# Performance work log

Hardware: AMD Instinct MI355X
Metric: run time of the kernel (lower is better)

## Reference

```python
import jax, jax.numpy as jnp
import numpy as np

D_MODEL = 1024
HEADS = 16
D_K = D_MODEL // HEADS
D_FF = 4096
B, S = 2, 2048
EPS = 1e-5


def setup_inputs() -> dict:
    key = jax.random.key(0)
    ks = jax.random.split(key, 16)
    sc_att = 1.0 / np.sqrt(D_MODEL)
    sc_ff1 = 1.0 / np.sqrt(D_MODEL)
    sc_ff2 = 1.0 / np.sqrt(D_FF)
    return {
        "input": jax.random.normal(ks[0], (B, S, D_MODEL), jnp.float32),
        "mask": jnp.ones((B, 1, 1, S), jnp.int32),
        # stacked per-head projections: [H, D_MODEL, D_K]
        "Wq": jax.random.normal(ks[1], (HEADS, D_MODEL, D_K), jnp.float32) * sc_att,
        "bq": jax.random.normal(ks[2], (HEADS, D_K), jnp.float32) * 0.01,
        "Wk": jax.random.normal(ks[3], (HEADS, D_MODEL, D_K), jnp.float32) * sc_att,
        "bk": jax.random.normal(ks[4], (HEADS, D_K), jnp.float32) * 0.01,
        "Wv": jax.random.normal(ks[5], (HEADS, D_MODEL, D_K), jnp.float32) * sc_att,
        "bv": jax.random.normal(ks[6], (HEADS, D_K), jnp.float32) * 0.01,
        "Wo": jax.random.normal(ks[7], (D_MODEL, D_MODEL), jnp.float32) * sc_att,
        "bo": jax.random.normal(ks[8], (D_MODEL,), jnp.float32) * 0.01,
        "ln1_g": jnp.ones((D_MODEL,), jnp.float32),
        "ln1_b": jnp.zeros((D_MODEL,), jnp.float32),
        "ln2_g": jnp.ones((D_MODEL,), jnp.float32),
        "ln2_b": jnp.zeros((D_MODEL,), jnp.float32),
        "W1": jax.random.normal(ks[9], (D_MODEL, D_FF), jnp.float32) * sc_ff1,
        "b1": jax.random.normal(ks[10], (D_FF,), jnp.float32) * 0.01,
        "W2": jax.random.normal(ks[11], (D_FF, D_MODEL), jnp.float32) * sc_ff2,
        "b2": jax.random.normal(ks[12], (D_MODEL,), jnp.float32) * 0.01,
    }


def _layernorm(x, g, b):
    mu = jnp.mean(x, axis=-1, keepdims=True)
    var = jnp.mean(jnp.square(x - mu), axis=-1, keepdims=True)
    return (x - mu) * jax.lax.rsqrt(var + EPS) * g + b


def reference(input, mask, Wq, bq, Wk, bk, Wv, bv, Wo, bo,
              ln1_g, ln1_b, ln2_g, ln2_b, W1, b1, W2, b2):
    x = input
    # per-head projections, stacked: [B,H,S,D_K]
    q = jnp.einsum('bsd,hdk->bhsk', x, Wq) + bq[None, :, None, :]
    k = jnp.einsum('bsd,hdk->bhsk', x, Wk) + bk[None, :, None, :]
    v = jnp.einsum('bsd,hdk->bhsk', x, Wv) + bv[None, :, None, :]
    scores = jnp.einsum('bhqk,bhsk->bhqs', q, k) / np.sqrt(D_K)  # [B,H,S,S]
    scores = jnp.where(mask == 0, jnp.float32(-1e9), scores)
    attn = jax.nn.softmax(scores, axis=-1)
    ctx = jnp.einsum('bhqs,bhsk->bhqk', attn, v)  # [B,H,S,D_K]
    # concat heads along feature dim (head h occupies slice h*D_K:(h+1)*D_K)
    ctx = jnp.transpose(ctx, (0, 2, 1, 3)).reshape(B, S, D_MODEL)
    att_out = ctx @ Wo + bo
    h = _layernorm(x + att_out, ln1_g, ln1_b)
    ff = jax.nn.relu(h @ W1 + b1) @ W2 + b2
    return _layernorm(h + ff, ln2_g, ln2_b)
```

## Files before the change

### kernel.cpp

```cpp
#include <hip/hip_runtime.h>
#include <cstdint>
#include <cstddef>

typedef unsigned short u16;
typedef unsigned int   u32;
typedef unsigned short u16x4 __attribute__((ext_vector_type(4)));
typedef unsigned short u16x8 __attribute__((ext_vector_type(8)));
typedef unsigned int   u32x2 __attribute__((ext_vector_type(2)));
typedef __bf16 bf16x8 __attribute__((ext_vector_type(8)));
typedef float f32x4 __attribute__((ext_vector_type(4)));

#define MFMA16(a, b, c) __builtin_amdgcn_mfma_f32_16x16x32_bf16((a), (b), (c), 0, 0, 0)
#define WAIT_VM0() __builtin_amdgcn_s_waitcnt(0x0F70)
#define BARRIER()  __builtin_amdgcn_s_barrier()

__device__ __forceinline__ float bf2f(u16 h) {
  union { unsigned u; float f; } v; v.u = ((unsigned)h) << 16; return v.f;
}
__device__ __forceinline__ u16 f2bf(float f) {
  union { float f; unsigned u; } v; v.f = f;
  unsigned r = v.u + 0x7fffu + ((v.u >> 16) & 1u);
  return (u16)(r >> 16);
}
__device__ __forceinline__ void gll16(const u16* g, u16* l) {
  __builtin_amdgcn_global_load_lds(
      (const __attribute__((address_space(1))) void*)g,
      (__attribute__((address_space(3))) void*)l, 16, 0, 0);
}
__device__ __forceinline__ float fast_exp2(float x) {
#if __has_builtin(__builtin_amdgcn_exp2f)
  return __builtin_amdgcn_exp2f(x);
#else
  return exp2f(x);
#endif
}

__global__ __launch_bounds__(256) void transpose_qkv(
    const float* __restrict__ Wq, const float* __restrict__ Wk,
    const float* __restrict__ Wv, u16* __restrict__ outb) {
  __shared__ u16 tile[32][33];
  const int z = blockIdx.z;
  const int which = z >> 4, h = z & 15;
  const float* in = (which == 0 ? Wq : (which == 1 ? Wk : Wv)) + (size_t)h * 1024 * 64;
  u16* out = outb + ((size_t)which * 1024 + h * 64) * 1024;
  const int tx = threadIdx.x & 31, ty = threadIdx.x >> 5;
  const int r0 = blockIdx.y * 32, c0 = blockIdx.x * 32;
  #pragma unroll
  for (int i = 0; i < 32; i += 8)
    tile[ty + i][tx] = f2bf(in[(size_t)(r0 + ty + i) * 64 + c0 + tx]);
  __syncthreads();
  #pragma unroll
  for (int i = 0; i < 32; i += 8)
    out[(size_t)(c0 + ty + i) * 1024 + r0 + tx] = tile[tx][ty + i];
}

__global__ __launch_bounds__(256) void transpose_w(
    const float* __restrict__ Wo, const float* __restrict__ W1,
    const float* __restrict__ W2, u16* __restrict__ Wo_t,
    u16* __restrict__ W1_t, u16* __restrict__ W2_t) {
  __shared__ u16 tile[32][33];
  const int id = blockIdx.x;
  const float* in; u16* outp; int R, C, cx, ry;
  if (id < 1024)      { in = Wo; outp = Wo_t; R = 1024; C = 1024; cx = id & 31;  ry = id >> 5; }
  else if (id < 5120) { int t = id - 1024; in = W1; outp = W1_t; R = 1024; C = 4096; cx = t & 127; ry = t >> 7; }
  else                { int t = id - 5120; in = W2; outp = W2_t; R = 4096; C = 1024; cx = t & 31;  ry = t >> 5; }
  const int tx = threadIdx.x & 31, ty = threadIdx.x >> 5;
  const int r0 = ry * 32, c0 = cx * 32;
  #pragma unroll
  for (int i = 0; i < 32; i += 8)
    tile[ty + i][tx] = f2bf(in[(size_t)(r0 + ty + i) * C + c0 + tx]);
  __syncthreads();
  #pragma unroll
  for (int i = 0; i < 32; i += 8)
    outp[(size_t)(c0 + ty + i) * R + r0 + tx] = tile[tx][ty + i];
}

__global__ __launch_bounds__(256) void prep_small(
    const float* __restrict__ bq, const float* __restrict__ bk,
    const float* __restrict__ bv, const int* __restrict__ mask,
    float* __restrict__ biasq, float* __restrict__ madd2) {
  int i = blockIdx.x * 256 + threadIdx.x;
  if (i < 3072) {
    biasq[i] = (i < 1024) ? bq[i] : (i < 2048 ? bk[i - 1024] : bv[i - 2048]);
  } else if (i < 7168) {
    int j = i - 3072;
    madd2[j] = mask[j] ? -23.083120f : -1.442695e9f;
  }
}

__global__ __launch_bounds__(256) void cvt_x(
    const float* __restrict__ in, u16* __restrict__ out, int n) {
  int i = (blockIdx.x * 256 + threadIdx.x) * 4;
  if (i >= n) return;
  const float4 v = *(const float4*)&in[i];
  u16x4 o;
  o[0] = f2bf(v.x); o[1] = f2bf(v.y); o[2] = f2bf(v.z); o[3] = f2bf(v.w);
  *(u16x4*)&out[i] = o;
}

template <int MODE>
__global__ __launch_bounds__(256) void gemm_bt(
    const u16* __restrict__ A, const u16* __restrict__ Bt,
    const float* __restrict__ bias, u16* __restrict__ C,
    int M, int N, int K) {
  __shared__ __align__(16) u16 As[2][128 * 32];
  __shared__ __align__(16) u16 Bs[2][128 * 32];
  const int tid = threadIdx.x;
  const int lane = tid & 63;
  const int wave = tid >> 6;
  const int m0 = blockIdx.y * 128;
  const int n0 = blockIdx.x * 128;
  const int kz = (MODE == 2) ? blockIdx.z : 0;
  const int Keff = (MODE == 2) ? (K >> 1) : K;
  const int kbase = kz * Keff;
  const int wr = (wave >> 1) * 64;
  const int wc = (wave & 1) * 64;
  const int lrow = lane & 15;
  const int quad = lane >> 4;

  const int srow = lane >> 2;
  const int scol = (lane & 3) * 8;
  const u16* gA1 = &A[(size_t)(m0 + wave * 16 + srow) * K + kbase + scol];
  const u16* gA2 = &A[(size_t)(m0 + 64 + wave * 16 + srow) * K + kbase + scol];
  const u16* gB1 = &Bt[(size_t)(n0 + wave * 16 + srow) * K + kbase + scol];
  const u16* gB2 = &Bt[(size_t)(n0 + 64 + wave * 16 + srow) * K + kbase + scol];
  const int so1 = (wave * 16) * 32;
  const int so2 = (wave * 16 + 64) * 32;
  u16* Cw = (MODE == 2) ? (C + (size_t)kz * M * N) : C;

  f32x4 acc[4][4];
  #pragma unroll
  for (int i = 0; i < 4; ++i)
    #pragma unroll
    for (int j = 0; j < 4; ++j)
      acc[i][j] = (f32x4){0.f, 0.f, 0.f, 0.f};

  gll16(gA1, &As[0][so1]);
  gll16(gA2, &As[0][so2]);
  gll16(gB1, &Bs[0][so1]);
  gll16(gB2, &Bs[0][so2]);

  const int nIter = Keff >> 5;
  for (int it = 0; it < nIter; ++it) {
    const int cur = it & 1;
    WAIT_VM0();
    BARRIER();
    const int k1 = (it + 1) << 5;
    if (k1 < Keff) {
      gll16(gA1 + k1, &As[cur ^ 1][so1]);
      gll16(gA2 + k1, &As[cur ^ 1][so2]);
      gll16(gB1 + k1, &Bs[cur ^ 1][so1]);
      gll16(gB2 + k1, &Bs[cur ^ 1][so2]);
    }
    bf16x8 af[4], bfr[4];
    #pragma unroll
    for (int i = 0; i < 4; ++i) {
      af[i]  = *(const bf16x8*)&As[cur][(wr + i * 16 + lrow) * 32 + quad * 8];
      bfr[i] = *(const bf16x8*)&Bs[cur][(wc + i * 16 + lrow) * 32 + quad * 8];
    }
    #pragma unroll
    for (int fr = 0; fr < 4; ++fr)
      #pragma unroll
      for (int fc = 0; fc < 4; ++fc)
        acc[fr][fc] = MFMA16(af[fr], bfr[fc], acc[fr][fc]);
  }

  #pragma unroll
  for (int fr = 0; fr < 4; ++fr) {
    int rowb = m0 + wr + fr * 16 + quad * 4;
    #pragma unroll
    for (int fc = 0; fc < 4; ++fc) {
      int col = n0 + wc + fc * 16 + lrow;
      float bv = (MODE == 2) ? 0.f : bias[col];
      #pragma unroll
      for (int r = 0; r < 4; ++r) {
        float v = acc[fr][fc][r] + bv;
        if (MODE == 1) v = fmaxf(v, 0.f);
        Cw[(size_t)(rowb + r) * N + col] = f2bf(v);
      }
    }
  }
}

__global__ __launch_bounds__(256) void attn_kernel(
    const u16* __restrict__ xqkv, const float* __restrict__ madd2,
    u16* __restrict__ opart, float* __restrict__ lpart) {
  __shared__ __align__(16) u16 Ks[64][72];
  __shared__ __align__(16) u16 Vt[64][136];
  __shared__ __align__(16) u16 Ps[4][2][16][72];
  const int tid = threadIdx.x;
  const int lane = tid & 63;
  const int wave = tid >> 6;
  const int lrow = lane & 15;
  const int quad = lane >> 4;
  const int b = blockIdx.z >> 1, kz = blockIdx.z & 1;
  const int h = blockIdx.y;
  const int qb = blockIdx.x * 128 + wave * 16;
  const u16* Qp = xqkv + (size_t)b * 2048 * 3072 + h * 64;
  const u16* Kp = Qp + 1024;
  const u16* Vp = Qp + 2048;
  const float S2 = 0.18033688f;
  const int sbeg = kz * 1024, send = sbeg + 1024;

  bf16x8 qa[2][2];
  #pragma unroll
  for (int t = 0; t < 2; ++t) {
    qa[t][0] = *(const bf16x8*)&Qp[(size_t)(qb + t * 64 + lrow) * 3072 + quad * 8];
    qa[t][1] = *(const bf16x8*)&Qp[(size_t)(qb + t * 64 + lrow) * 3072 + 32 + quad * 8];
  }

  f32x4 o[2][4];
  #pragma unroll
  for (int t = 0; t < 2; ++t)
    #pragma unroll
    for (int i = 0; i < 4; ++i) o[t][i] = (f32x4){0.f, 0.f, 0.f, 0.f};
  float rsum[2] = {0.f, 0.f};

  const int ks_row = tid >> 3, ks_col = (tid & 7) * 8;
  const int v_dg = tid >> 4;
  const int v_kp = tid & 15;
  const float* maddb = madd2 + b * 2048;

  u16x8 kreg[2];
  u16x4 va[2], vb[2];
  #pragma unroll
  for (int sh = 0; sh < 2; ++sh) {
    kreg[sh] = *(const u16x8*)&Kp[(size_t)(sbeg + sh * 32 + ks_row) * 3072 + ks_col];
    va[sh] = *(const u16x4*)&Vp[(size_t)(sbeg + sh * 32 + 2 * v_kp) * 3072 + v_dg * 4];
    vb[sh] = *(const u16x4*)&Vp[(size_t)(sbeg + sh * 32 + 2 * v_kp + 1) * 3072 + v_dg * 4];
  }

  for (int s0 = sbeg; s0 < send; s0 += 64) {
    __syncthreads();
    #pragma unroll
    for (int sh = 0; sh < 2; ++sh) {
      *(u16x8*)&Ks[sh * 32 + ks_row][ks_col] = kreg[sh];
      #pragma unroll
      for (int j = 0; j < 4; ++j) {
        u32 pk = ((u32)vb[sh][j] << 16) | (u32)va[sh][j];
        *(u32*)&Vt[v_dg * 4 + j][sh * 32 + 2 * v_kp] = pk;
      }
    }
    __syncthreads();
    if (s0 + 64 < send) {
      #pragma unroll
      for (int sh = 0; sh < 2; ++sh) {
        int sb = s0 + 64 + sh * 32;
        kreg[sh] = *(const u16x8*)&Kp[(size_t)(sb + ks_row) * 3072 + ks_col];
        va[sh] = *(const u16x4*)&Vp[(size_t)(sb + 2 * v_kp) * 3072 + v_dg * 4];
        vb[sh] = *(const u16x4*)&Vp[(size_t)(sb + 2 * v_kp + 1) * 3072 + v_dg * 4];
      }
    }

    bf16x8 kf[4][2], vf[4][2];
    #pragma unroll
    for (int kb = 0; kb < 4; ++kb) {
      kf[kb][0] = *(const bf16x8*)&Ks[kb * 16 + lrow][quad * 8];
      kf[kb][1] = *(const bf16x8*)&Ks[kb * 16 + lrow][32 + quad * 8];
    }
    #pragma unroll
    for (int nb = 0; nb < 4; ++nb) {
      vf[nb][0] = *(const bf16x8*)&Vt[nb * 16 + lrow][quad * 8];
      vf[nb][1] = *(const bf16x8*)&Vt[nb * 16 + lrow][32 + quad * 8];
    }

    #pragma unroll
    for (int t = 0; t < 2; ++t) {
      #pragma unroll
      for (int kb = 0; kb < 4; ++kb) {
        f32x4 z = (f32x4){0.f, 0.f, 0.f, 0.f};
        z = MFMA16(kf[kb][0], qa[t][0], z);
        z = MFMA16(kf[kb][1], qa[t][1], z);
        f32x4 m4 = *(const f32x4*)&maddb[s0 + kb * 16 + quad * 4];
        u32 pb[4];
        #pragma unroll
        for (int r = 0; r < 4; ++r) {
          float p = fast_exp2(fmaf(z[r], S2, m4[r]));
          rsum[t] += p;
          union { float f; u32 u; } cv; cv.f = p;
          pb[r] = cv.u + 0x8000u;
        }
        u32x2 w2;
        w2[0] = __builtin_amdgcn_perm(pb[1], pb[0], 0x07060302);
        w2[1] = __builtin_amdgcn_perm(pb[3], pb[2], 0x07060302);
        *(u32x2*)&Ps[wave][t][lrow][kb * 16 + quad * 4] = w2;
      }
      #pragma unroll
      for (int kh = 0; kh < 2; ++kh) {
        bf16x8 pa = *(const bf16x8*)&Ps[wave][t][lrow][kh * 32 + quad * 8];
        #pragma unroll
        for (int nb = 0; nb < 4; ++nb)
          o[t][nb] = MFMA16(pa, vf[nb][kh], o[t][nb]);
      }
    }
  }

  u16* ob = opart + (size_t)kz * 4194304;
  float* lb = lpart + (size_t)kz * 65536 + ((size_t)b * 16 + h) * 2048;
  #pragma unroll
  for (int t = 0; t < 2; ++t) {
    float rs = rsum[t];
    rs += __shfl_xor(rs, 16, 64);
    rs += __shfl_xor(rs, 32, 64);
    if (lane < 16) lb[qb + t * 64 + lane] = rs;
    #pragma unroll
    for (int r = 0; r < 4; ++r) {
      int q = qb + t * 64 + quad * 4 + r;
      #pragma unroll
      for (int nb = 0; nb < 4; ++nb)
        ob[((size_t)b * 2048 + q) * 1024 + h * 64 + nb * 16 + lrow] =
            f2bf(o[t][nb][r]);
    }
  }
}

__global__ __launch_bounds__(256) void attn_combine(
    const u16* __restrict__ opart, const float* __restrict__ lpart,
    u16* __restrict__ ctx) {
  const int t = blockIdx.x;
  const int b = t >> 11, q = t & 2047;
  const int tid = threadIdx.x;
  const size_t base = (size_t)t * 1024;
  #pragma unroll
  for (int i = 0; i < 4; ++i) {
    int c = i * 256 + tid;
    int h = c >> 6;
    float l = lpart[((size_t)b * 16 + h) * 2048 + q] +
              lpart[65536 + ((size_t)b * 16 + h) * 2048 + q];
    float o = bf2f(opart[base + c]) + bf2f(opart[4194304 + base + c]);
    ctx[base + c] = f2bf(o / fmaxf(l, 1e-30f));
  }
}

template <int IN_BF, int OUT_BF>
__global__ __launch_bounds__(256) void add_ln2p(
    const void* __restrict__ xa_, const u16* __restrict__ p0,
    const u16* __restrict__ p1, const float* __restrict__ cb,
    const float* __restrict__ g, const float* __restrict__ bb,
    void* __restrict__ outp_) {
  __shared__ float red[8];
  const int tid = threadIdx.x;
  const size_t base = (size_t)blockIdx.x * 1024;
  const float* xf = (const float*)xa_;
  const u16*   xb = (const u16*)xa_;
  float v[4];
  float s = 0.f;
  #pragma unroll
  for (int i = 0; i < 4; ++i) {
    int c = i * 256 + tid;
    float xv = IN_BF ? bf2f(xb[base + c]) : xf[base + c];
    v[i] = xv + bf2f(p0[base + c]) + bf2f(p1[base + c]) + cb[c];
    s += v[i];
  }
  #pragma unroll
  for (int off = 32; off > 0; off >>= 1) s += __shfl_down(s, off, 64);
  if ((tid & 63) == 0) red[tid >> 6] = s;
  __syncthreads();
  float mean = (red[0] + red[1] + red[2] + red[3]) * (1.f / 1024.f);
  float s2 = 0.f;
  #pragma unroll
  for (int i = 0; i < 4; ++i) { float d = v[i] - mean; s2 += d * d; }
  #pragma unroll
  for (int off = 32; off > 0; off >>= 1) s2 += __shfl_down(s2, off, 64);
  if ((tid & 63) == 0) red[4 + (tid >> 6)] = s2;
  __syncthreads();
  float var = (red[4] + red[5] + red[6] + red[7]) * (1.f / 1024.f);
  float rstd = rsqrtf(var + 1e-5f);
  #pragma unroll
  for (int i = 0; i < 4; ++i) {
    int c = i * 256 + tid;
    float r = (v[i] - mean) * rstd * g[c] + bb[c];
    if (OUT_BF) ((u16*)outp_)[base + c] = f2bf(r);
    else        ((float*)outp_)[base + c] = r;
  }
}

extern "C" void kernel_launch(void* const* d_in, const int* in_sizes, int n_in,
                              void* d_out, int out_size, void* d_ws, size_t ws_size,
                              hipStream_t stream) {
  (void)in_sizes; (void)n_in; (void)out_size; (void)ws_size;
  const float* x    = (const float*)d_in[0];
  const int*   mask = (const int*)d_in[1];
  const float* Wq   = (const float*)d_in[2];
  const float* bq   = (const float*)d_in[3];
  const float* Wk   = (const float*)d_in[4];
  const float* bk   = (const float*)d_in[5];
  const float* Wv   = (const float*)d_in[6];
  const float* bv   = (const float*)d_in[7];
  const float* Wo   = (const float*)d_in[8];
  const float* bo   = (const float*)d_in[9];
  const float* ln1g = (const float*)d_in[10];
  const float* ln1b = (const float*)d_in[11];
  const float* ln2g = (const float*)d_in[12];
  const float* ln2b = (const float*)d_in[13];
  const float* W1   = (const float*)d_in[14];
  const float* b1   = (const float*)d_in[15];
  const float* W2   = (const float*)d_in[16];
  const float* b2   = (const float*)d_in[17];
  float* out = (float*)d_out;

  char* ws = (char*)d_ws;
  float* lpart  = (float*)(ws + 0);
  u16*   fp     = (u16*)(ws + 0);
  u16*   Wqkv_t = (u16*)(ws + 0);
  u16*   Wo_t   = (u16*)(ws + 6291456);
  u16*   W1_t   = (u16*)(ws + 8388608);
  u16*   W2_t   = (u16*)(ws + 16777216);
  u16*   xqkv   = (u16*)(ws + 25165824);
  u16*   wp     = (u16*)(ws + 25165824);
  u16*   xb     = (u16*)(ws + 50331648);
  u16*   ctx    = (u16*)(ws + 50331648);
  u16*   opart  = (u16*)(ws + 58720256);
  u16*   hbuf   = (u16*)(ws + 58720256);
  u16*   ff1    = (u16*)(ws + 25165824);
  float* biasq  = (float*)(ws + 75497472);
  float* madd2  = (float*)(ws + 75509760);

  prep_small<<<28, 256, 0, stream>>>(bq, bk, bv, mask, biasq, madd2);
  transpose_qkv<<<dim3(2, 32, 48), 256, 0, stream>>>(Wq, Wk, Wv, Wqkv_t);
  transpose_w<<<9216, 256, 0, stream>>>(Wo, W1, W2, Wo_t, W1_t, W2_t);
  cvt_x<<<4096, 256, 0, stream>>>(x, xb, 4194304);

  gemm_bt<0><<<dim3(24, 32), 256, 0, stream>>>(xb, Wqkv_t, biasq, xqkv,
                                               4096, 3072, 1024);
  attn_kernel<<<dim3(16, 16, 4), 256, 0, stream>>>(xqkv, madd2, opart, lpart);
  attn_combine<<<4096, 256, 0, stream>>>(opart, lpart, ctx);
  gemm_bt<2><<<dim3(8, 32, 2), 256, 0, stream>>>(ctx, Wo_t, nullptr, wp,
                                                 4096, 1024, 1024);
  add_ln2p<0, 1><<<4096, 256, 0, stream>>>(x, wp, wp + 4194304, bo,
                                           ln1g, ln1b, hbuf);
  gemm_bt<1><<<dim3(32, 32), 256, 0, stream>>>(hbuf, W1_t, b1, ff1,
                                               4096, 4096, 1024);
  gemm_bt<2><<<dim3(8, 32, 2), 256, 0, stream>>>(ff1, W2_t, nullptr, fp,
                                                 4096, 1024, 4096);
  add_ln2p<1, 0><<<4096, 256, 0, stream>>>(hbuf, fp, fp + 4194304, b2,
                                           ln2g, ln2b, out);
}
```

Measured before the change: 383.1 us.

## Merge weight transposes, add 64-row QKV GEMM, drop split-K attention combine

Merges the two weight-transpose kernels into a single launch. Adds a smaller-tile 64x128 GEMM for the QKV projection, which gives more blocks for occupancy. Changes attention to process the full key range per block and normalize in-kernel, which removes the partial-output buffers and the separate combine kernel. The cost is half as many attention blocks (512 instead of 1024), each doing twice the sequential work, so parallelism drops on a GPU with many CUs.

```diff
diff --git a/kernel.cpp b/kernel.cpp
--- a/kernel.cpp
+++ b/kernel.cpp
@@ -35,35 +35,31 @@
 #endif
 }
 
-__global__ __launch_bounds__(256) void transpose_qkv(
+__global__ __launch_bounds__(256) void transpose_all(
     const float* __restrict__ Wq, const float* __restrict__ Wk,
-    const float* __restrict__ Wv, u16* __restrict__ outb) {
-  __shared__ u16 tile[32][33];
-  const int z = blockIdx.z;
-  const int which = z >> 4, h = z & 15;
-  const float* in = (which == 0 ? Wq : (which == 1 ? Wk : Wv)) + (size_t)h * 1024 * 64;
-  u16* out = outb + ((size_t)which * 1024 + h * 64) * 1024;
-  const int tx = threadIdx.x & 31, ty = threadIdx.x >> 5;
-  const int r0 = blockIdx.y * 32, c0 = blockIdx.x * 32;
-  #pragma unroll
-  for (int i = 0; i < 32; i += 8)
-    tile[ty + i][tx] = f2bf(in[(size_t)(r0 + ty + i) * 64 + c0 + tx]);
-  __syncthreads();
-  #pragma unroll
-  for (int i = 0; i < 32; i += 8)
-    out[(size_t)(c0 + ty + i) * 1024 + r0 + tx] = tile[tx][ty + i];
-}
-
-__global__ __launch_bounds__(256) void transpose_w(
-    const float* __restrict__ Wo, const float* __restrict__ W1,
-    const float* __restrict__ W2, u16* __restrict__ Wo_t,
+    const float* __restrict__ Wv, const float* __restrict__ Wo,
+    const float* __restrict__ W1, const float* __restrict__ W2,
+    u16* __restrict__ Wqkv_t, u16* __restrict__ Wo_t,
     u16* __restrict__ W1_t, u16* __restrict__ W2_t) {
   __shared__ u16 tile[32][33];
   const int id = blockIdx.x;
   const float* in; u16* outp; int R, C, cx, ry;
-  if (id < 1024)      { in = Wo; outp = Wo_t; R = 1024; C = 1024; cx = id & 31;  ry = id >> 5; }
-  else if (id < 5120) { int t = id - 1024; in = W1; outp = W1_t; R = 1024; C = 4096; cx = t & 127; ry = t >> 7; }
-  else                { int t = id - 5120; in = W2; outp = W2_t; R = 4096; C = 1024; cx = t & 31;  ry = t >> 5; }
+  if (id < 3072) {
+    int z = id >> 6, t = id & 63;
+    int which = z >> 4, h = z & 15;
+    in = (which == 0 ? Wq : (which == 1 ? Wk : Wv)) + (size_t)h * 1024 * 64;
+    outp = Wqkv_t + ((size_t)which * 1024 + h * 64) * 1024;
+    R = 1024; C = 64; cx = t & 1; ry = t >> 1;
+  } else if (id < 4096) {
+    int t = id - 3072; in = Wo; outp = Wo_t;
+    R = 1024; C = 1024; cx = t & 31; ry = t >> 5;
+  } else if (id < 8192) {
+    int t = id - 4096; in = W1; outp = W1_t;
+    R = 1024; C = 4096; cx = t & 127; ry = t >> 7;
+  } else {
+    int t = id - 8192; in = W2; outp = W2_t;
+    R = 4096; C = 1024; cx = t & 31; ry = t >> 5;
+  }
   const int tx = threadIdx.x & 31, ty = threadIdx.x >> 5;
   const int r0 = ry * 32, c0 = cx * 32;
   #pragma unroll
@@ -182,9 +178,85 @@
   }
 }
 
+__global__ __launch_bounds__(256) void gemm64_bt(
+    const u16* __restrict__ A, const u16* __restrict__ Bt,
+    const float* __restrict__ bias, u16* __restrict__ C,
+    int M, int N, int K) {
+  __shared__ __align__(16) u16 As[2][64 * 32];
+  __shared__ __align__(16) u16 Bs[2][128 * 32];
+  const int tid = threadIdx.x;
+  const int lane = tid & 63;
+  const int wave = tid >> 6;
+  const int m0 = blockIdx.y * 64;
+  const int n0 = blockIdx.x * 128;
+  const int wr = (wave >> 1) * 32;
+  const int wc = (wave & 1) * 64;
+  const int lrow = lane & 15;
+  const int quad = lane >> 4;
+
+  const int srow = lane >> 2;
+  const int scol = (lane & 3) * 8;
+  const u16* gA1 = &A[(size_t)(m0 + wave * 16 + srow) * K + scol];
+  const u16* gB1 = &Bt[(size_t)(n0 + wave * 16 + srow) * K + scol];
+  const u16* gB2 = &Bt[(size_t)(n0 + 64 + wave * 16 + srow) * K + scol];
+  const int so1 = (wave * 16) * 32;
+  const int so2 = (wave * 16 + 64) * 32;
+
+  f32x4 acc[2][4];
+  #pragma unroll
+  for (int i = 0; i < 2; ++i)
+    #pragma unroll
+    for (int j = 0; j < 4; ++j)
+      acc[i][j] = (f32x4){0.f, 0.f, 0.f, 0.f};
+
+  gll16(gA1, &As[0][so1]);
+  gll16(gB1, &Bs[0][so1]);
+  gll16(gB2, &Bs[0][so2]);
+
+  const int nIter = K >> 5;
+  for (int it = 0; it < nIter; ++it) {
+    const int cur = it & 1;
+    WAIT_VM0();
+    BARRIER();
+    const int k1 = (it + 1) << 5;
+    if (k1 < K) {
+      gll16(gA1 + k1, &As[cur ^ 1][so1]);
+      gll16(gB1 + k1, &Bs[cur ^ 1][so1]);
+      gll16(gB2 + k1, &Bs[cur ^ 1][so2]);
+    }
+    bf16x8 af[2], bfr[4];
+    #pragma unroll
+    for (int i = 0; i < 2; ++i)
+      af[i] = *(const bf16x8*)&As[cur][(wr + i * 16 + lrow) * 32 + quad * 8];
+    #pragma unroll
+    for (int j = 0; j < 4; ++j)
+      bfr[j] = *(const bf16x8*)&Bs[cur][(wc + j * 16 + lrow) * 32 + quad * 8];
+    #pragma unroll
+    for (int fr = 0; fr < 2; ++fr)
+      #pragma unroll
+      for (int fc = 0; fc < 4; ++fc)
+        acc[fr][fc] = MFMA16(af[fr], bfr[fc], acc[fr][fc]);
+  }
+
+  #pragma unroll
+  for (int fr = 0; fr < 2; ++fr) {
+    int rowb = m0 + wr + fr * 16 + quad * 4;
+    #pragma unroll
+    for (int fc = 0; fc < 4; ++fc) {
+      int col = n0 + wc + fc * 16 + lrow;
+      float bv = bias[col];
+      #pragma unroll
+      for (int r = 0; r < 4; ++r) {
+        float v = acc[fr][fc][r] + bv;
+        C[(size_t)(rowb + r) * N + col] = f2bf(v);
+      }
+    }
+  }
+}
+
 __global__ __launch_bounds__(256) void attn_kernel(
     const u16* __restrict__ xqkv, const float* __restrict__ madd2,
-    u16* __restrict__ opart, float* __restrict__ lpart) {
+    u16* __restrict__ ctx) {
   __shared__ __align__(16) u16 Ks[64][72];
   __shared__ __align__(16) u16 Vt[64][136];
   __shared__ __align__(16) u16 Ps[4][2][16][72];
@@ -193,14 +265,12 @@
   const int wave = tid >> 6;
   const int lrow = lane & 15;
   const int quad = lane >> 4;
-  const int b = blockIdx.z >> 1, kz = blockIdx.z & 1;
-  const int h = blockIdx.y;
+  const int b = blockIdx.z, h = blockIdx.y;
   const int qb = blockIdx.x * 128 + wave * 16;
   const u16* Qp = xqkv + (size_t)b * 2048 * 3072 + h * 64;
   const u16* Kp = Qp + 1024;
   const u16* Vp = Qp + 2048;
   const float S2 = 0.18033688f;
-  const int sbeg = kz * 1024, send = sbeg + 1024;
 
   bf16x8 qa[2][2];
   #pragma unroll
@@ -225,12 +295,12 @@
   u16x4 va[2], vb[2];
   #pragma unroll
   for (int sh = 0; sh < 2; ++sh) {
-    kreg[sh] = *(const u16x8*)&Kp[(size_t)(sbeg + sh * 32 + ks_row) * 3072 + ks_col];
-    va[sh] = *(const u16x4*)&Vp[(size_t)(sbeg + sh * 32 + 2 * v_kp) * 3072 + v_dg * 4];
-    vb[sh] = *(const u16x4*)&Vp[(size_t)(sbeg + sh * 32 + 2 * v_kp + 1) * 3072 + v_dg * 4];
-  }
-
-  for (int s0 = sbeg; s0 < send; s0 += 64) {
+    kreg[sh] = *(const u16x8*)&Kp[(size_t)(sh * 32 + ks_row) * 3072 + ks_col];
+    va[sh] = *(const u16x4*)&Vp[(size_t)(sh * 32 + 2 * v_kp) * 3072 + v_dg * 4];
+    vb[sh] = *(const u16x4*)&Vp[(size_t)(sh * 32 + 2 * v_kp + 1) * 3072 + v_dg * 4];
+  }
+
+  for (int s0 = 0; s0 < 2048; s0 += 64) {
     __syncthreads();
     #pragma unroll
     for (int sh = 0; sh < 2; ++sh) {
@@ -242,7 +312,7 @@
       }
     }
     __syncthreads();
-    if (s0 + 64 < send) {
+    if (s0 + 64 < 2048) {
       #pragma unroll
       for (int sh = 0; sh < 2; ++sh) {
         int sb = s0 + 64 + sh * 32;
@@ -295,40 +365,22 @@
     }
   }
 
-  u16* ob = opart + (size_t)kz * 4194304;
-  float* lb = lpart + (size_t)kz * 65536 + ((size_t)b * 16 + h) * 2048;
   #pragma unroll
   for (int t = 0; t < 2; ++t) {
     float rs = rsum[t];
     rs += __shfl_xor(rs, 16, 64);
     rs += __shfl_xor(rs, 32, 64);
-    if (lane < 16) lb[qb + t * 64 + lane] = rs;
+    float inv = 1.f / fmaxf(rs, 1e-30f);
     #pragma unroll
     for (int r = 0; r < 4; ++r) {
+      float invq = __shfl(inv, quad * 4 + r, 64);
       int q = qb + t * 64 + quad * 4 + r;
       #pragma unroll
-      for (int nb = 0; nb < 4; ++nb)
-        ob[((size_t)b * 2048 + q) * 1024 + h * 64 + nb * 16 + lrow] =
-            f2bf(o[t][nb][r]);
-    }
-  }
-}
-
-__global__ __launch_bounds__(256) void attn_combine(
-    const u16* __restrict__ opart, const float* __restrict__ lpart,
-    u16* __restrict__ ctx) {
-  const int t = blockIdx.x;
-  const int b = t >> 11, q = t & 2047;
-  const int tid = threadIdx.x;
-  const size_t base = (size_t)t * 1024;
-  #pragma unroll
-  for (int i = 0; i < 4; ++i) {
-    int c = i * 256 + tid;
-    int h = c >> 6;
-    float l = lpart[((size_t)b * 16 + h) * 2048 + q] +
-              lpart[65536 + ((size_t)b * 16 + h) * 2048 + q];
-    float o = bf2f(opart[base + c]) + bf2f(opart[4194304 + base + c]);
-    ctx[base + c] = f2bf(o / fmaxf(l, 1e-30f));
+      for (int nb = 0; nb < 4; ++nb) {
+        float v = o[t][nb][r] * invq;
+        ctx[((size_t)b * 2048 + q) * 1024 + h * 64 + nb * 16 + lrow] = f2bf(v);
+      }
+    }
   }
 }
 
@@ -400,9 +452,8 @@
   float* out = (float*)d_out;
 
   char* ws = (char*)d_ws;
-  float* lpart  = (float*)(ws + 0);
+  u16*   Wqkv_t = (u16*)(ws + 0);
   u16*   fp     = (u16*)(ws + 0);
-  u16*   Wqkv_t = (u16*)(ws + 0);
   u16*   Wo_t   = (u16*)(ws + 6291456);
   u16*   W1_t   = (u16*)(ws + 8388608);
   u16*   W2_t   = (u16*)(ws + 16777216);
@@ -410,21 +461,19 @@
   u16*   wp     = (u16*)(ws + 25165824);
   u16*   xb     = (u16*)(ws + 50331648);
   u16*   ctx    = (u16*)(ws + 50331648);
-  u16*   opart  = (u16*)(ws + 58720256);
+  u16*   ff1    = (u16*)(ws + 25165824);
   u16*   hbuf   = (u16*)(ws + 58720256);
-  u16*   ff1    = (u16*)(ws + 25165824);
   float* biasq  = (float*)(ws + 75497472);
   float* madd2  = (float*)(ws + 75509760);
 
   prep_small<<<28, 256, 0, stream>>>(bq, bk, bv, mask, biasq, madd2);
-  transpose_qkv<<<dim3(2, 32, 48), 256, 0, stream>>>(Wq, Wk, Wv, Wqkv_t);
-  transpose_w<<<9216, 256, 0, stream>>>(Wo, W1, W2, Wo_t, W1_t, W2_t);
+  transpose_all<<<12288, 256, 0, stream>>>(Wq, Wk, Wv, Wo, W1, W2,
+                                           Wqkv_t, Wo_t, W1_t, W2_t);
   cvt_x<<<4096, 256, 0, stream>>>(x, xb, 4194304);
 
-  gemm_bt<0><<<dim3(24, 32), 256, 0, stream>>>(xb, Wqkv_t, biasq, xqkv,
-                                               4096, 3072, 1024);
-  attn_kernel<<<dim3(16, 16, 4), 256, 0, stream>>>(xqkv, madd2, opart, lpart);
-  attn_combine<<<4096, 256, 0, stream>>>(opart, lpart, ctx);
+  gemm64_bt<<<dim3(24, 64), 256, 0, stream>>>(xb, Wqkv_t, biasq, xqkv,
+                                              4096, 3072, 1024);
+  attn_kernel<<<dim3(16, 16, 2), 256, 0, stream>>>(xqkv, madd2, ctx);
   gemm_bt<2><<<dim3(8, 32, 2), 256, 0, stream>>>(ctx, Wo_t, nullptr, wp,
                                                  4096, 1024, 1024);
   add_ln2p<0, 1><<<4096, 256, 0, stream>>>(x, wp, wp + 4194304, bo,
```

Result: no change. 386.9 us (+1.0%).
